# Kernel tuning notes

Hardware: AMD Instinct MI355X
Metric: run time of the kernel (lower is better)

Reference implementation:

```python
import jax, jax.numpy as jnp
import numpy as np

VIS_DIM, VIS_NUM, EMBED, HIDDEN, VOCAB = 512, 196, 256, 512, 10000
B, T = 128, 20


def setup_inputs() -> dict:
    key = jax.random.key(0)
    ks = jax.random.split(key, 16)
    s = 0.02
    return {
        "features": jax.random.normal(ks[0], (B, VIS_NUM, VIS_DIM), jnp.float32),
        "captions": jax.random.randint(ks[1], (B, T), 0, VOCAB),
        "W_init_h": jax.random.normal(ks[2], (HIDDEN, VIS_DIM), jnp.float32) * s,
        "W_init_c": jax.random.normal(ks[3], (HIDDEN, VIS_DIM), jnp.float32) * s,
        "Wv": jax.random.normal(ks[4], (1, VIS_DIM), jnp.float32) * s,
        "bv": jnp.zeros((1,), jnp.float32),
        "Wa": jax.random.normal(ks[5], (1, HIDDEN), jnp.float32) * s,
        "ba": jnp.zeros((1,), jnp.float32),
        "embed_table": jax.random.normal(ks[6], (VOCAB, EMBED), jnp.float32) * s,
        "W_ih": jax.random.normal(ks[7], (4 * HIDDEN, VIS_DIM + EMBED), jnp.float32) * s,
        "W_hh": jax.random.normal(ks[8], (4 * HIDDEN, HIDDEN), jnp.float32) * s,
        "b_ih": jnp.zeros((4 * HIDDEN,), jnp.float32),
        "b_hh": jnp.zeros((4 * HIDDEN,), jnp.float32),
        "Wo": jax.random.normal(ks[9], (VOCAB, HIDDEN), jnp.float32) * s,
        "bo": jnp.zeros((VOCAB,), jnp.float32),
    }


def reference(features, captions, W_init_h, W_init_c, Wv, bv, Wa, ba,
              embed_table, W_ih, W_hh, b_ih, b_hh, Wo, bo):
    b, t = captions.shape
    vis_num = features.shape[1]
    # _init_hidden: sum over spatial locations of a bias-free linear, / vis_num
    h0 = jnp.sum(jnp.einsum('bnv,hv->bnh', features, W_init_h), axis=1) / vis_num  # [B,H]
    c0 = jnp.sum(jnp.einsum('bnv,hv->bnh', features, W_init_c), axis=1) / vis_num  # [B,H]
    emb = embed_table[captions]  # [B,T,E]
    # visual part of attention logits is constant across timesteps
    att_v = jnp.einsum('bnv,ov->bno', features, Wv) + bv  # [B,N,1]

    def step(carry, emb_t):
        h, c = carry
        att = att_v + (h @ Wa.T + ba)[:, None, :]          # [B,N,1]
        alpha = jax.nn.softmax(att, axis=1)                # softmax over vis_num
        ctx = jnp.sum(features * alpha, axis=1)            # [B,vis_dim]
        x = jnp.concatenate([ctx, emb_t], axis=1)          # [B,vis_dim+E]
        gates = x @ W_ih.T + b_ih + h @ W_hh.T + b_hh      # [B,4H]
        i, f, g, o = jnp.split(gates, 4, axis=1)           # torch LSTM gate order
        i, f, o = jax.nn.sigmoid(i), jax.nn.sigmoid(f), jax.nn.sigmoid(o)
        g = jnp.tanh(g)
        c = f * c + i * g
        h = o * jnp.tanh(c)
        words = h @ Wo.T + bo                              # [B,V]
        return (h, c), words

    (_, _), ws = jax.lax.scan(step, (h0, c0), jnp.swapaxes(emb, 0, 1))  # [T,B,V]
    # pack_padded_sequence (all lengths = T, batch_first) yields time-major [T*B, V]
    flat = ws.reshape(t * b, -1)
    return jax.nn.log_softmax(flat, axis=1), jax.nn.softmax(flat, axis=1)
```

## Files before the change

kernel.cpp:

```cpp
#include <hip/hip_runtime.h>

typedef unsigned short u16;
typedef unsigned int u32;
typedef unsigned long long u64;

typedef __attribute__((ext_vector_type(8))) short short8;
typedef __attribute__((ext_vector_type(4))) float float4v;

__device__ __forceinline__ float bf2f(u16 u) { return __uint_as_float(((u32)u) << 16); }
__device__ __forceinline__ u16 f2bf(float f) {
    u32 x = __float_as_uint(f);
    return (u16)((x + 0x7fffu + ((x >> 16) & 1u)) >> 16);
}
__device__ __forceinline__ float sigmoidf_(float x) { return 1.0f / (1.0f + expf(-x)); }

#define B_ 128
#define T_ 20
#define VISN 196
#define VISD 512
#define EMB 256
#define HID 512
#define VOC 10000
#define VOCP 10112
#define NBLK 64


__global__ __launch_bounds__(256) void conv_all(
    const float* __restrict__ Wih, const float* __restrict__ Whh,
    const float* __restrict__ Wo,  const float* __restrict__ Winh,
    const float* __restrict__ Winc, const float* __restrict__ bih,
    const float* __restrict__ bhh, const float* __restrict__ bo,
    u16* __restrict__ cWih, u16* __restrict__ cWhh, u16* __restrict__ cWo,
    u16* __restrict__ cWinit, u16* __restrict__ cbih, u16* __restrict__ cbhh,
    u16* __restrict__ cbo, int* __restrict__ flags) {
    const int e0 = 1572864, e1 = 2621440, e2 = 7798784, e3 = 8060928,
              e4 = 8323072, e5 = 8325120, e6 = 8327168, e7 = 8337280;
    int gid = blockIdx.x * 256 + threadIdx.x;
    if (gid < 256) flags[gid] = 0;
    if (gid >= e7) return;
    if (gid < e0) { cWih[gid] = f2bf(Wih[gid]); }
    else if (gid < e1) { int l = gid - e0; cWhh[l] = f2bf(Whh[l]); }
    else if (gid < e2) {
        int l = gid - e1; int row = l >> 9, col = l & 511;
        cWo[l] = (row < VOC) ? f2bf(Wo[(size_t)row * 512 + col]) : (u16)0;
    }
    else if (gid < e3) { int l = gid - e2; cWinit[l] = f2bf(Winh[l]); }
    else if (gid < e4) { int l = gid - e3; cWinit[262144 + l] = f2bf(Winc[l]); }
    else if (gid < e5) { int l = gid - e4; cbih[l] = f2bf(bih[l]); }
    else if (gid < e6) { int l = gid - e5; cbhh[l] = f2bf(bhh[l]); }
    else { int l = gid - e6; cbo[l] = (l < VOC) ? f2bf(bo[l]) : (u16)0; }
}

__global__ __launch_bounds__(256) void att_kernel(const float* __restrict__ feat,
                                                  const float* __restrict__ Wv,
                                                  float* __restrict__ alpha) {
    __shared__ float wv[512];
    __shared__ float att[VISN];
    __shared__ float red[256];
    int b = blockIdx.x, tid = threadIdx.x;
    wv[tid] = Wv[tid];
    wv[tid + 256] = Wv[tid + 256];
    __syncthreads();
    int w = tid >> 6, lane = tid & 63;
    for (int n = w; n < VISN; n += 4) {
        const float4* fp = (const float4*)(feat + ((size_t)b * VISN + n) * VISD) + lane * 2;
        float4 a = fp[0], c = fp[1];
        const float* wp = wv + lane * 8;
        float s = a.x * wp[0] + a.y * wp[1] + a.z * wp[2] + a.w * wp[3]
                + c.x * wp[4] + c.y * wp[5] + c.z * wp[6] + c.w * wp[7];
        #pragma unroll
        for (int off = 32; off; off >>= 1) s += __shfl_down(s, off);
        if (lane == 0) att[n] = s;
    }
    __syncthreads();
    float m = -1e30f;
    for (int i = tid; i < VISN; i += 256) m = fmaxf(m, att[i]);
    red[tid] = m; __syncthreads();
    for (int s = 128; s; s >>= 1) { if (tid < s) red[tid] = fmaxf(red[tid], red[tid + s]); __syncthreads(); }
    m = red[0]; __syncthreads();
    float sum = 0.f;
    for (int i = tid; i < VISN; i += 256) { float e = expf(att[i] - m); att[i] = e; sum += e; }
    red[tid] = sum; __syncthreads();
    for (int s = 128; s; s >>= 1) { if (tid < s) red[tid] += red[tid + s]; __syncthreads(); }
    float inv = 1.0f / red[0]; __syncthreads();
    for (int i = tid; i < VISN; i += 256) alpha[b * VISN + i] = att[i] * inv;
}

__global__ __launch_bounds__(256) void ctx_fbar(const float* __restrict__ feat,
                                                const float* __restrict__ alpha,
                                                u16* __restrict__ fbar_bf,
                                                u16* __restrict__ ctx_bf) {
    __shared__ float al[VISN];
    int b = blockIdx.y, tid = threadIdx.x;
    int v = blockIdx.x * 256 + tid;
    if (tid < VISN) al[tid] = alpha[b * VISN + tid];
    __syncthreads();
    float accf = 0.f, accc = 0.f;
    const float* fp = feat + (size_t)b * VISN * VISD + v;
    #pragma unroll 4
    for (int n = 0; n < VISN; n++) {
        float f = fp[(size_t)n * VISD];
        accf += f;
        accc += al[n] * f;
    }
    fbar_bf[b * VISD + v] = f2bf(accf / (float)VISN);
    ctx_bf[b * VISD + v] = f2bf(accc);
}

__global__ void gather_emb(const int* __restrict__ captions, const float* __restrict__ table,
                           u16* __restrict__ Ebf) {
    int r = blockIdx.x;
    int t = r >> 7, b = r & 127;
    int idx = captions[b * T_ + t];
    Ebf[(size_t)r * EMB + threadIdx.x] = f2bf(table[(size_t)idx * EMB + threadIdx.x]);
}

__global__ __launch_bounds__(256) void gemm_bt(const u16* __restrict__ A, int lda,
                                               const u16* __restrict__ Bm, int ldb,
                                               int M, int N, int K,
                                               const u16* __restrict__ bias0,
                                               const u16* __restrict__ bias1,
                                               const float* __restrict__ addA, int rowmask,
                                               float* __restrict__ Cf,
                                               u16* __restrict__ Cbf, int ldc, int mode) {
    __shared__ u16 As[64 * 32];
    __shared__ u16 Bs[64 * 32];
    int tid = threadIdx.x;
    int n0 = blockIdx.x * 64, m0 = blockIdx.y * 64;
    int w = tid >> 6, lane = tid & 63;
    int wm = (w & 1) * 32, wn = (w >> 1) * 32;
    int mrow = lane & 15, quad = lane >> 4;
    float4v acc[2][2] = {};
    int lr = tid >> 2;
    int lc = (tid & 3) * 8;
    for (int k0 = 0; k0 < K; k0 += 32) {
        *(uint4*)(&As[lr * 32 + lc]) = *(const uint4*)(A + (size_t)(m0 + lr) * lda + k0 + lc);
        *(uint4*)(&Bs[lr * 32 + lc]) = *(const uint4*)(Bm + (size_t)(n0 + lr) * ldb + k0 + lc);
        __syncthreads();
        short8 afrag[2], bfrag[2];
        #pragma unroll
        for (int i = 0; i < 2; i++)
            afrag[i] = *(const short8*)(&As[(wm + i * 16 + mrow) * 32 + quad * 8]);
        #pragma unroll
        for (int j = 0; j < 2; j++)
            bfrag[j] = *(const short8*)(&Bs[(wn + j * 16 + mrow) * 32 + quad * 8]);
        #pragma unroll
        for (int i = 0; i < 2; i++)
            #pragma unroll
            for (int j = 0; j < 2; j++)
                acc[i][j] = __builtin_amdgcn_mfma_f32_16x16x32_bf16(afrag[i], bfrag[j], acc[i][j], 0, 0, 0);
        __syncthreads();
    }
    #pragma unroll
    for (int i = 0; i < 2; i++) {
        #pragma unroll
        for (int j = 0; j < 2; j++) {
            #pragma unroll
            for (int r = 0; r < 4; r++) {
                int grow = m0 + wm + i * 16 + quad * 4 + r;
                int gcol = n0 + wn + j * 16 + mrow;
                float v = acc[i][j][r];
                if (bias0) v += bf2f(bias0[gcol]);
                if (bias1) v += bf2f(bias1[gcol]);
                if (addA) v += addA[(size_t)(grow & rowmask) * ldc + gcol];
                if (mode == 0) {
                    Cbf[(size_t)grow * ldc + gcol] = f2bf(v);
                } else if (mode == 1) {
                    Cf[(size_t)grow * ldc + gcol] = v;
                } else {
                    if (gcol < 512) {
                        size_t o = ((((size_t)(grow >> 4) * 16 + (gcol >> 5)) * 4 +
                                     ((gcol >> 3) & 3)) * 16 + (grow & 15)) * 8 + (gcol & 7);
                        Cbf[o] = f2bf(v);
                    } else {
                        Cf[(size_t)grow * 512 + gcol - 512] = v;
                    }
                }
            }
        }
    }
}

__global__ __launch_bounds__(256, 1) void recurrence(
    const u16* __restrict__ Whh,
    const float* __restrict__ gbase,
    const float* __restrict__ c0,
    u16* __restrict__ h_pp,
    u16* __restrict__ h_all,
    int* __restrict__ flags) {
    __shared__ u16 Ws[64 * 520];
    __shared__ __align__(16) u16 ex[64 * 16];
    int jb = blockIdx.x, tid = threadIdx.x;
    int rg = jb >> 5, cg = jb & 31;
    for (int idx = tid; idx < 64 * 64; idx += 256) {
        int lcol = idx >> 6, q8 = idx & 63;
        int grow = ((lcol >> 4) << 9) + (cg << 4) + (lcol & 15);
        *(uint4*)&Ws[lcol * 520 + q8 * 8] = *(const uint4*)&Whh[(size_t)grow * 512 + q8 * 8];
    }
    int w = tid >> 6, lane = tid & 63;
    int mrow = lane & 15, quad = lane >> 4;
    int rowC = (rg << 6) + (w << 4) + (quad << 2);
    int strip = (rg << 2) + w;
    int colh = (cg << 4) + mrow;
    float cst[4];
    #pragma unroll
    for (int r = 0; r < 4; r++) cst[r] = c0[(size_t)(rowC + r) * 512 + colh];
    __syncthreads();
    short8 bfv[16][4];
    #pragma unroll
    for (int ks = 0; ks < 16; ks++)
        #pragma unroll
        for (int g = 0; g < 4; g++)
            bfv[ks][g] = *(const short8*)&Ws[((g << 4) + mrow) * 520 + ks * 32 + quad * 8];
    for (int t = 0; t < T_; t++) {
        const u64* hb64 = (const u64*)(h_pp + (t & 1) * 65536);
        u16* hnxt = h_pp + ((t + 1) & 1) * 65536;
        float gb[4][4];
        #pragma unroll
        for (int g = 0; g < 4; g++)
            #pragma unroll
            for (int r = 0; r < 4; r++)
                gb[g][r] = gbase[(size_t)(t * B_ + rowC + r) * 2048 + (g << 9) + colh];
        if (t > 0) {
            if (tid < 32) {
                int pj = (rg << 5) + tid;
                int fi = ((pj & 15) << 4) + (pj >> 4);
                while (__hip_atomic_load(&flags[fi], __ATOMIC_RELAXED,
                                         __HIP_MEMORY_SCOPE_AGENT) < t)
                    __builtin_amdgcn_s_sleep(1);
            }
            __syncthreads();
        }
        short8 af[16];
        #pragma unroll
        for (int ks = 0; ks < 16; ks++) {
            int o = (((strip * 16 + ks) * 4 + quad) * 16 + mrow) * 2;
            union { u64 q[2]; short8 v; } uu;
            uu.q[0] = __hip_atomic_load(hb64 + o, __ATOMIC_RELAXED,
                                        __HIP_MEMORY_SCOPE_AGENT);
            uu.q[1] = __hip_atomic_load(hb64 + o + 1, __ATOMIC_RELAXED,
                                        __HIP_MEMORY_SCOPE_AGENT);
            af[ks] = uu.v;
        }
        float4v acc[4] = {};
        #pragma unroll
        for (int ks = 0; ks < 16; ks++)
            #pragma unroll
            for (int g = 0; g < 4; g++)
                acc[g] = __builtin_amdgcn_mfma_f32_16x16x32_bf16(af[ks], bfv[ks][g], acc[g], 0, 0, 0);
        #pragma unroll
        for (int r = 0; r < 4; r++) {
            float ig = sigmoidf_(acc[0][r] + gb[0][r]);
            float fg = sigmoidf_(acc[1][r] + gb[1][r]);
            float gg = tanhf(acc[2][r] + gb[2][r]);
            float og = sigmoidf_(acc[3][r] + gb[3][r]);
            float cn = fg * cst[r] + ig * gg;
            cst[r] = cn;
            ex[((w << 4) + (quad << 2) + r) * 16 + mrow] = f2bf(og * tanhf(cn));
        }
        __syncthreads();
        const u32* ex32 = (const u32*)ex;
        #pragma unroll
        for (int h2 = 0; h2 < 2; h2++) {
            int d = tid + h2 * 256;
            int c = d >> 6, i = d & 63;
            int wl = c >> 1, qs = c & 1, mw = i >> 2, ep = i & 3;
            u32 val = ex32[((wl * 16 + mw) * 16 + qs * 8 + ep * 2) >> 1];
            size_t o16 = ((((size_t)((rg << 2) + wl) * 16 + (cg >> 1)) * 4 +
                          ((cg & 1) * 2 + qs)) * 16 + mw) * 8 + ep * 2;
            __hip_atomic_store((u32*)hnxt + (o16 >> 1), val,
                               __ATOMIC_RELAXED, __HIP_MEMORY_SCOPE_AGENT);
        }
        if (tid < 128) {
            int rl = tid >> 1, hf = tid & 1;
            uint4 v = *(const uint4*)&ex[rl * 16 + hf * 8];
            *(uint4*)&h_all[(size_t)(t * B_ + (rg << 6) + rl) * 512 + (cg << 4) + hf * 8] = v;
        }
        asm volatile("s_waitcnt vmcnt(0)" ::: "memory");
        __syncthreads();
        if (tid == 0) {
            int fi = ((jb & 15) << 4) + (jb >> 4);
            __hip_atomic_store(&flags[fi], t + 1, __ATOMIC_RELAXED,
                               __HIP_MEMORY_SCOPE_AGENT);
        }
    }
}

__global__ __launch_bounds__(256) void gemm128(const u16* __restrict__ A,
                                               const u16* __restrict__ Bm,
                                               const u16* __restrict__ biasbf,
                                               float* __restrict__ C) {
    __shared__ u16 As[128 * 32];
    __shared__ u16 Bs[128 * 32];
    int tid = threadIdx.x;
    int n0 = blockIdx.x * 128, m0 = blockIdx.y * 128;
    int w = tid >> 6, lane = tid & 63;
    int wm = (w & 1) * 64, wn = (w >> 1) * 64;
    int mrow = lane & 15, quad = lane >> 4;
    float4v acc[4][4] = {};
    for (int k0 = 0; k0 < 512; k0 += 32) {
        #pragma unroll
        for (int q = 0; q < 2; q++) {
            int idx = tid * 2 + q;
            int r = idx >> 2, cc = (idx & 3) * 8;
            *(uint4*)&As[r * 32 + cc] = *(const uint4*)&A[(size_t)(m0 + r) * 512 + k0 + cc];
            *(uint4*)&Bs[r * 32 + cc] = *(const uint4*)&Bm[(size_t)(n0 + r) * 512 + k0 + cc];
        }
        __syncthreads();
        short8 af[4], bfv[4];
        #pragma unroll
        for (int i = 0; i < 4; i++)
            af[i] = *(const short8*)&As[(wm + i * 16 + mrow) * 32 + quad * 8];
        #pragma unroll
        for (int jn = 0; jn < 4; jn++)
            bfv[jn] = *(const short8*)&Bs[(wn + jn * 16 + mrow) * 32 + quad * 8];
        #pragma unroll
        for (int i = 0; i < 4; i++)
            #pragma unroll
            for (int jn = 0; jn < 4; jn++)
                acc[i][jn] = __builtin_amdgcn_mfma_f32_16x16x32_bf16(af[i], bfv[jn], acc[i][jn], 0, 0, 0);
        __syncthreads();
    }
    #pragma unroll
    for (int i = 0; i < 4; i++) {
        #pragma unroll
        for (int jn = 0; jn < 4; jn++) {
            int gcol = n0 + wn + jn * 16 + mrow;
            if (gcol >= VOC) continue;
            float bias = bf2f(biasbf[gcol]);
            #pragma unroll
            for (int r = 0; r < 4; r++) {
                int grow = m0 + wm + i * 16 + quad * 4 + r;
                C[(size_t)grow * VOC + gcol] = acc[i][jn][r] + bias;
            }
        }
    }
}

__global__ __launch_bounds__(256) void softmax_out(float* __restrict__ out) {
    __shared__ float red[256];
    int r = blockIdx.x, tid = threadIdx.x;
    const size_t HALF4 = (size_t)T_ * B_ * VOC / 4;
    float4* outv = (float4*)out;
    float4* src = outv + HALF4 + (size_t)r * (VOC / 4);
    float4 lv[10];
    float m = -1e30f;
    #pragma unroll
    for (int jq = 0; jq < 10; jq++) {
        int i4 = tid + jq * 256;
        if (i4 < VOC / 4) {
            float4 v = src[i4];
            lv[jq] = v;
            m = fmaxf(m, fmaxf(fmaxf(v.x, v.y), fmaxf(v.z, v.w)));
        } else {
            lv[jq] = make_float4(-1e30f, -1e30f, -1e30f, -1e30f);
        }
    }
    red[tid] = m; __syncthreads();
    for (int s = 128; s; s >>= 1) { if (tid < s) red[tid] = fmaxf(red[tid], red[tid + s]); __syncthreads(); }
    m = red[0]; __syncthreads();
    float sum = 0.f;
    #pragma unroll
    for (int jq = 0; jq < 10; jq++)
        sum += expf(lv[jq].x - m) + expf(lv[jq].y - m) + expf(lv[jq].z - m) + expf(lv[jq].w - m);
    red[tid] = sum; __syncthreads();
    for (int s = 128; s; s >>= 1) { if (tid < s) red[tid] += red[tid + s]; __syncthreads(); }
    float logZ = m + logf(red[0]);
    float4* dls = outv + (size_t)r * (VOC / 4);
    #pragma unroll
    for (int jq = 0; jq < 10; jq++) {
        int i4 = tid + jq * 256;
        if (i4 < VOC / 4) {
            float4 v = lv[jq];
            float4 ls = make_float4(v.x - logZ, v.y - logZ, v.z - logZ, v.w - logZ);
            dls[i4] = ls;
            src[i4] = make_float4(expf(ls.x), expf(ls.y), expf(ls.z), expf(ls.w));
        }
    }
}

extern "C" void kernel_launch(void* const* d_in, const int* in_sizes, int n_in,
                              void* d_out, int out_size, void* d_ws, size_t ws_size,
                              hipStream_t stream) {
    const float* features = (const float*)d_in[0];
    const int* captions   = (const int*)d_in[1];
    const float* W_init_h = (const float*)d_in[2];
    const float* W_init_c = (const float*)d_in[3];
    const float* Wv       = (const float*)d_in[4];
    const float* embed_t  = (const float*)d_in[8];
    const float* W_ih     = (const float*)d_in[9];
    const float* W_hh     = (const float*)d_in[10];
    const float* b_ih     = (const float*)d_in[11];
    const float* b_hh     = (const float*)d_in[12];
    const float* Wo       = (const float*)d_in[13];
    const float* bo       = (const float*)d_in[14];
    float* out = (float*)d_out;

    char* base = (char*)d_ws;
    int*   flags   = (int*)(base + 0);
    float* alpha   = (float*)(base + 1024);
    u16*   fbar_bf = (u16*)(base + 103424);
    u16*   ctx_bf  = (u16*)(base + 234496);
    u16*   h_pp    = (u16*)(base + 365568);
    float* c_f32   = (float*)(base + 627712);
    float* gconst  = (float*)(base + 889856);
    u16*   Ebf     = (u16*)(base + 1938432);
    float* gbase   = (float*)(base + 3249152);
    u16*   h_all   = (u16*)(base + 24220672);
    u16*   cWih    = (u16*)(base + 26842112);
    u16*   cWhh    = (u16*)(base + 29987840);
    u16*   cWo     = (u16*)(base + 32084992);
    u16*   cWinit  = (u16*)(base + 42439680);
    u16*   cbih    = (u16*)(base + 43488256);
    u16*   cbhh    = (u16*)(base + 43492352);
    u16*   cbo     = (u16*)(base + 43496448);

    conv_all<<<32568, 256, 0, stream>>>(W_ih, W_hh, Wo, W_init_h, W_init_c,
                                        b_ih, b_hh, bo,
                                        cWih, cWhh, cWo, cWinit, cbih, cbhh, cbo, flags);
    att_kernel<<<B_, 256, 0, stream>>>(features, Wv, alpha);
    ctx_fbar<<<dim3(2, B_), 256, 0, stream>>>(features, alpha, fbar_bf, ctx_bf);
    gather_emb<<<T_ * B_, 256, 0, stream>>>(captions, embed_t, Ebf);
    gemm_bt<<<dim3(16, 2), 256, 0, stream>>>(
        fbar_bf, 512, cWinit, 512, B_, 1024, 512,
        nullptr, nullptr, nullptr, -1, c_f32, h_pp, 1024, 2);
    gemm_bt<<<dim3(32, 2), 256, 0, stream>>>(
        ctx_bf, 512, cWih, 768, B_, 2048, 512,
        cbih, cbhh, nullptr, -1, gconst, nullptr, 2048, 1);
    gemm_bt<<<dim3(32, 40), 256, 0, stream>>>(
        Ebf, 256, cWih + 512, 768, T_ * B_, 2048, 256,
        nullptr, nullptr, gconst, 127, gbase, nullptr, 2048, 1);
    recurrence<<<NBLK, 256, 0, stream>>>(cWhh, gbase, c_f32, h_pp, h_all, flags);
    gemm128<<<dim3(VOCP / 128, (T_ * B_) / 128), 256, 0, stream>>>(
        h_all, cWo, cbo, out + (size_t)T_ * B_ * VOC);
    softmax_out<<<T_ * B_, 256, 0, stream>>>(out);
}
```

Baseline: 583.8 us.

## Fuse preprocessing kernels, pad LDS tiles, and signal recurrence flags earlier

Folds the embedding gather into the weight-conversion kernel and merges the attention softmax with the context/mean reduction into one per-batch kernel, removing two launches and the alpha round trip through global memory. Pads the shared-memory tile row stride from 32 to 40 elements in both GEMMs to reduce LDS bank conflicts on fragment reads. In the recurrence, the per-step flag is published before the h_all store instead of after it, which shortens the critical path between blocks. The fused att_ctx runs only 128 blocks, each covering the full feature row, so the context pass has less parallelism than the previous 256-block launch.

```diff
diff --git a/kernel.cpp b/kernel.cpp
--- a/kernel.cpp
+++ b/kernel.cpp
@@ -23,6 +23,7 @@
 #define VOC 10000
 #define VOCP 10112
 #define NBLK 64
+#define LDP 40
 
 
 __global__ __launch_bounds__(256) void conv_all(
@@ -30,14 +31,16 @@
     const float* __restrict__ Wo,  const float* __restrict__ Winh,
     const float* __restrict__ Winc, const float* __restrict__ bih,
     const float* __restrict__ bhh, const float* __restrict__ bo,
+    const int* __restrict__ captions, const float* __restrict__ table,
     u16* __restrict__ cWih, u16* __restrict__ cWhh, u16* __restrict__ cWo,
     u16* __restrict__ cWinit, u16* __restrict__ cbih, u16* __restrict__ cbhh,
-    u16* __restrict__ cbo, int* __restrict__ flags) {
+    u16* __restrict__ cbo, u16* __restrict__ Ebf, int* __restrict__ flags) {
     const int e0 = 1572864, e1 = 2621440, e2 = 7798784, e3 = 8060928,
-              e4 = 8323072, e5 = 8325120, e6 = 8327168, e7 = 8337280;
+              e4 = 8323072, e5 = 8325120, e6 = 8327168, e7 = 8337280,
+              e8 = 8992640;
     int gid = blockIdx.x * 256 + threadIdx.x;
     if (gid < 256) flags[gid] = 0;
-    if (gid >= e7) return;
+    if (gid >= e8) return;
     if (gid < e0) { cWih[gid] = f2bf(Wih[gid]); }
     else if (gid < e1) { int l = gid - e0; cWhh[l] = f2bf(Whh[l]); }
     else if (gid < e2) {
@@ -48,12 +51,19 @@
     else if (gid < e4) { int l = gid - e3; cWinit[262144 + l] = f2bf(Winc[l]); }
     else if (gid < e5) { int l = gid - e4; cbih[l] = f2bf(bih[l]); }
     else if (gid < e6) { int l = gid - e5; cbhh[l] = f2bf(bhh[l]); }
-    else { int l = gid - e6; cbo[l] = (l < VOC) ? f2bf(bo[l]) : (u16)0; }
-}
-
-__global__ __launch_bounds__(256) void att_kernel(const float* __restrict__ feat,
-                                                  const float* __restrict__ Wv,
-                                                  float* __restrict__ alpha) {
+    else if (gid < e7) { int l = gid - e6; cbo[l] = (l < VOC) ? f2bf(bo[l]) : (u16)0; }
+    else {
+        int l = gid - e7; int r = l >> 8, col = l & 255;
+        int t = r >> 7, b = r & 127;
+        int idx = captions[b * T_ + t];
+        Ebf[(size_t)r * EMB + col] = f2bf(table[(size_t)idx * EMB + col]);
+    }
+}
+
+__global__ __launch_bounds__(256) void att_ctx(const float* __restrict__ feat,
+                                               const float* __restrict__ Wv,
+                                               u16* __restrict__ fbar_bf,
+                                               u16* __restrict__ ctx_bf) {
     __shared__ float wv[512];
     __shared__ float att[VISN];
     __shared__ float red[256];
@@ -83,36 +93,22 @@
     red[tid] = sum; __syncthreads();
     for (int s = 128; s; s >>= 1) { if (tid < s) red[tid] += red[tid + s]; __syncthreads(); }
     float inv = 1.0f / red[0]; __syncthreads();
-    for (int i = tid; i < VISN; i += 256) alpha[b * VISN + i] = att[i] * inv;
-}
-
-__global__ __launch_bounds__(256) void ctx_fbar(const float* __restrict__ feat,
-                                                const float* __restrict__ alpha,
-                                                u16* __restrict__ fbar_bf,
-                                                u16* __restrict__ ctx_bf) {
-    __shared__ float al[VISN];
-    int b = blockIdx.y, tid = threadIdx.x;
-    int v = blockIdx.x * 256 + tid;
-    if (tid < VISN) al[tid] = alpha[b * VISN + tid];
+    for (int i = tid; i < VISN; i += 256) att[i] *= inv;
     __syncthreads();
-    float accf = 0.f, accc = 0.f;
-    const float* fp = feat + (size_t)b * VISN * VISD + v;
-    #pragma unroll 4
-    for (int n = 0; n < VISN; n++) {
-        float f = fp[(size_t)n * VISD];
-        accf += f;
-        accc += al[n] * f;
-    }
-    fbar_bf[b * VISD + v] = f2bf(accf / (float)VISN);
-    ctx_bf[b * VISD + v] = f2bf(accc);
-}
-
-__global__ void gather_emb(const int* __restrict__ captions, const float* __restrict__ table,
-                           u16* __restrict__ Ebf) {
-    int r = blockIdx.x;
-    int t = r >> 7, b = r & 127;
-    int idx = captions[b * T_ + t];
-    Ebf[(size_t)r * EMB + threadIdx.x] = f2bf(table[(size_t)idx * EMB + threadIdx.x]);
+    #pragma unroll
+    for (int half = 0; half < 2; half++) {
+        int v = (half << 8) + tid;
+        float accf = 0.f, accc = 0.f;
+        const float* fp = feat + (size_t)b * VISN * VISD + v;
+        #pragma unroll 4
+        for (int n = 0; n < VISN; n++) {
+            float f = fp[(size_t)n * VISD];
+            accf += f;
+            accc += att[n] * f;
+        }
+        fbar_bf[b * VISD + v] = f2bf(accf / (float)VISN);
+        ctx_bf[b * VISD + v] = f2bf(accc);
+    }
 }
 
 __global__ __launch_bounds__(256) void gemm_bt(const u16* __restrict__ A, int lda,
@@ -123,8 +119,8 @@
                                                const float* __restrict__ addA, int rowmask,
                                                float* __restrict__ Cf,
                                                u16* __restrict__ Cbf, int ldc, int mode) {
-    __shared__ u16 As[64 * 32];
-    __shared__ u16 Bs[64 * 32];
+    __shared__ u16 As[64 * LDP];
+    __shared__ u16 Bs[64 * LDP];
     int tid = threadIdx.x;
     int n0 = blockIdx.x * 64, m0 = blockIdx.y * 64;
     int w = tid >> 6, lane = tid & 63;
@@ -134,16 +130,16 @@
     int lr = tid >> 2;
     int lc = (tid & 3) * 8;
     for (int k0 = 0; k0 < K; k0 += 32) {
-        *(uint4*)(&As[lr * 32 + lc]) = *(const uint4*)(A + (size_t)(m0 + lr) * lda + k0 + lc);
-        *(uint4*)(&Bs[lr * 32 + lc]) = *(const uint4*)(Bm + (size_t)(n0 + lr) * ldb + k0 + lc);
+        *(uint4*)(&As[lr * LDP + lc]) = *(const uint4*)(A + (size_t)(m0 + lr) * lda + k0 + lc);
+        *(uint4*)(&Bs[lr * LDP + lc]) = *(const uint4*)(Bm + (size_t)(n0 + lr) * ldb + k0 + lc);
         __syncthreads();
         short8 afrag[2], bfrag[2];
         #pragma unroll
         for (int i = 0; i < 2; i++)
-            afrag[i] = *(const short8*)(&As[(wm + i * 16 + mrow) * 32 + quad * 8]);
+            afrag[i] = *(const short8*)(&As[(wm + i * 16 + mrow) * LDP + quad * 8]);
         #pragma unroll
         for (int j = 0; j < 2; j++)
-            bfrag[j] = *(const short8*)(&Bs[(wn + j * 16 + mrow) * 32 + quad * 8]);
+            bfrag[j] = *(const short8*)(&Bs[(wn + j * 16 + mrow) * LDP + quad * 8]);
         #pragma unroll
         for (int i = 0; i < 2; i++)
             #pragma unroll
@@ -271,18 +267,18 @@
             __hip_atomic_store((u32*)hnxt + (o16 >> 1), val,
                                __ATOMIC_RELAXED, __HIP_MEMORY_SCOPE_AGENT);
         }
+        asm volatile("s_waitcnt vmcnt(0)" ::: "memory");
+        __syncthreads();
+        if (tid == 0) {
+            int fi = ((jb & 15) << 4) + (jb >> 4);
+            __hip_atomic_store(&flags[fi], t + 1, __ATOMIC_RELAXED,
+                               __HIP_MEMORY_SCOPE_AGENT);
+        }
         if (tid < 128) {
             int rl = tid >> 1, hf = tid & 1;
             uint4 v = *(const uint4*)&ex[rl * 16 + hf * 8];
             *(uint4*)&h_all[(size_t)(t * B_ + (rg << 6) + rl) * 512 + (cg << 4) + hf * 8] = v;
         }
-        asm volatile("s_waitcnt vmcnt(0)" ::: "memory");
-        __syncthreads();
-        if (tid == 0) {
-            int fi = ((jb & 15) << 4) + (jb >> 4);
-            __hip_atomic_store(&flags[fi], t + 1, __ATOMIC_RELAXED,
-                               __HIP_MEMORY_SCOPE_AGENT);
-        }
     }
 }
 
@@ -290,8 +286,8 @@
                                                const u16* __restrict__ Bm,
                                                const u16* __restrict__ biasbf,
                                                float* __restrict__ C) {
-    __shared__ u16 As[128 * 32];
-    __shared__ u16 Bs[128 * 32];
+    __shared__ u16 As[128 * LDP];
+    __shared__ u16 Bs[128 * LDP];
     int tid = threadIdx.x;
     int n0 = blockIdx.x * 128, m0 = blockIdx.y * 128;
     int w = tid >> 6, lane = tid & 63;
@@ -303,17 +299,17 @@
         for (int q = 0; q < 2; q++) {
             int idx = tid * 2 + q;
             int r = idx >> 2, cc = (idx & 3) * 8;
-            *(uint4*)&As[r * 32 + cc] = *(const uint4*)&A[(size_t)(m0 + r) * 512 + k0 + cc];
-            *(uint4*)&Bs[r * 32 + cc] = *(const uint4*)&Bm[(size_t)(n0 + r) * 512 + k0 + cc];
+            *(uint4*)&As[r * LDP + cc] = *(const uint4*)&A[(size_t)(m0 + r) * 512 + k0 + cc];
+            *(uint4*)&Bs[r * LDP + cc] = *(const uint4*)&Bm[(size_t)(n0 + r) * 512 + k0 + cc];
         }
         __syncthreads();
         short8 af[4], bfv[4];
         #pragma unroll
         for (int i = 0; i < 4; i++)
-            af[i] = *(const short8*)&As[(wm + i * 16 + mrow) * 32 + quad * 8];
+            af[i] = *(const short8*)&As[(wm + i * 16 + mrow) * LDP + quad * 8];
         #pragma unroll
         for (int jn = 0; jn < 4; jn++)
-            bfv[jn] = *(const short8*)&Bs[(wn + jn * 16 + mrow) * 32 + quad * 8];
+            bfv[jn] = *(const short8*)&Bs[(wn + jn * 16 + mrow) * LDP + quad * 8];
         #pragma unroll
         for (int i = 0; i < 4; i++)
             #pragma unroll
@@ -398,7 +394,6 @@
 
     char* base = (char*)d_ws;
     int*   flags   = (int*)(base + 0);
-    float* alpha   = (float*)(base + 1024);
     u16*   fbar_bf = (u16*)(base + 103424);
     u16*   ctx_bf  = (u16*)(base + 234496);
     u16*   h_pp    = (u16*)(base + 365568);
@@ -415,12 +410,11 @@
     u16*   cbhh    = (u16*)(base + 43492352);
     u16*   cbo     = (u16*)(base + 43496448);
 
-    conv_all<<<32568, 256, 0, stream>>>(W_ih, W_hh, Wo, W_init_h, W_init_c,
-                                        b_ih, b_hh, bo,
-                                        cWih, cWhh, cWo, cWinit, cbih, cbhh, cbo, flags);
-    att_kernel<<<B_, 256, 0, stream>>>(features, Wv, alpha);
-    ctx_fbar<<<dim3(2, B_), 256, 0, stream>>>(features, alpha, fbar_bf, ctx_bf);
-    gather_emb<<<T_ * B_, 256, 0, stream>>>(captions, embed_t, Ebf);
+    conv_all<<<35128, 256, 0, stream>>>(W_ih, W_hh, Wo, W_init_h, W_init_c,
+                                        b_ih, b_hh, bo, captions, embed_t,
+                                        cWih, cWhh, cWo, cWinit, cbih, cbhh, cbo,
+                                        Ebf, flags);
+    att_ctx<<<B_, 256, 0, stream>>>(features, Wv, fbar_bf, ctx_bf);
     gemm_bt<<<dim3(16, 2), 256, 0, stream>>>(
         fbar_bf, 512, cWinit, 512, B_, 1024, 512,
         nullptr, nullptr, nullptr, -1, c_f32, h_pp, 1024, 2);
```

Measured after the change: 597.5 us. +2.4%, slower.
